# Performance work log

Hardware: AMD Instinct MI355X
Metric: run time of the kernel (lower is better)

## Reference

```python
import jax, jax.numpy as jnp
import numpy as np

T = 11          # entity types
N_ENT = 100000  # entity nodes per type (= NUM_ENTITY_NODES embedding rows)
N_TX = 100000   # transaction nodes (must be <= N_ENT per original code's dst indexing)
D = 128         # hidden_dim (heads=1, concat -> out dim D)
E = 500000      # edges per entity type
F = 394         # tx_feature_dim
NEG_SLOPE = 0.2 # PyG GATConv default
LN_EPS = 1e-5


def _layernorm(x, gamma, beta):
    mu = jnp.mean(x, axis=-1, keepdims=True)
    var = jnp.mean((x - mu) ** 2, axis=-1, keepdims=True)
    return (x - mu) * jax.lax.rsqrt(var + LN_EPS) * gamma + beta


def setup_inputs():
    key = jax.random.key(0)
    ks = jax.random.split(key, 12)
    tx_x = jax.random.normal(ks[0], (N_TX, F), jnp.float32)
    entity_idx = jax.random.randint(ks[1], (T, N_ENT), 0, N_ENT, jnp.int32)
    edge_src = jax.random.randint(ks[2], (T, E), 0, N_ENT, jnp.int32)
    edge_dst = jax.random.randint(ks[3], (T, E), 0, min(N_ENT, N_TX), jnp.int32)
    emb_tables = jax.random.normal(ks[4], (T, N_ENT, D), jnp.float32)
    lin_w = jax.random.normal(ks[5], (D, D), jnp.float32) / np.float32(np.sqrt(D))
    att_src = jax.random.normal(ks[6], (D,), jnp.float32) / np.float32(np.sqrt(D))
    att_dst = jax.random.normal(ks[7], (D,), jnp.float32) / np.float32(np.sqrt(D))
    conv_bias = jnp.zeros((D,), jnp.float32)
    ln_gamma = jnp.ones((T, D), jnp.float32)
    ln_beta = jnp.zeros((T, D), jnp.float32)
    c_in = F + T * D  # classifier input: tx features + 11 entity messages
    w1 = jax.random.normal(ks[8], (c_in, D), jnp.float32) / np.float32(np.sqrt(c_in))
    b1 = jnp.zeros((D,), jnp.float32)
    w2 = jax.random.normal(ks[9], (D, 64), jnp.float32) / np.float32(np.sqrt(D))
    b2 = jnp.zeros((64,), jnp.float32)
    w3 = jax.random.normal(ks[10], (64, 1), jnp.float32) / np.float32(np.sqrt(64))
    b3 = jnp.zeros((1,), jnp.float32)
    return dict(tx_x=tx_x, emb_tables=emb_tables, lin_w=lin_w, att_src=att_src,
                att_dst=att_dst, conv_bias=conv_bias, ln_gamma=ln_gamma, ln_beta=ln_beta,
                w1=w1, b1=b1, w2=w2, b2=b2, w3=w3, b3=b3,
                entity_idx=entity_idx, edge_src=edge_src, edge_dst=edge_dst)


def _forward(tx_x, emb_tables, lin_w, att_src, att_dst, conv_bias, ln_gamma, ln_beta,
             w1, b1, w2, b2, w3, b3, entity_idx, edge_src, edge_dst):
    n_tx = tx_x.shape[0]
    loops = jnp.arange(N_ENT, dtype=edge_src.dtype)  # PyG GATConv add_self_loops=True
    msgs = []
    for t in range(T):  # fixed small set of entity types; GATConv weights shared (convs[0])
        x = emb_tables[t][entity_idx[t]]            # [N_ENT, D] embedding gather
        xw = x @ lin_w                              # GATConv linear (bias=False)
        a_s = xw @ att_src                          # [N_ENT] per-node src attention logit
        a_d = xw @ att_dst
        src, dst = edge_src[t], edge_dst[t]
        s_full = jnp.concatenate([src, loops])      # edges + self loops
        d_full = jnp.concatenate([dst, loops])
        e = jax.nn.leaky_relu(a_s[s_full] + a_d[d_full], NEG_SLOPE)
        # numerically stable edge softmax grouped by dst node
        m = jax.ops.segment_max(e, d_full, num_segments=N_ENT)
        ex = jnp.exp(e - m[d_full])
        denom = jax.ops.segment_sum(ex, d_full, num_segments=N_ENT)
        alpha = ex / (denom[d_full] + 1e-16)
        out = jax.ops.segment_sum(alpha[:, None] * xw[s_full], d_full,
                                  num_segments=N_ENT) + conv_bias  # [N_ENT, D]
        h = _layernorm(out, ln_gamma[t], ln_beta[t])
        # index_add_ scatter of h[src] into transaction rows (original edges only)
        agg = jnp.zeros((n_tx, D), h.dtype).at[dst].add(h[src])
        msgs.append(agg)
    combined = jnp.concatenate([tx_x] + msgs, axis=-1)  # [N_TX, F + T*D]
    h1 = jax.nn.relu(combined @ w1 + b1)
    h2 = jax.nn.relu(h1 @ w2 + b2)
    return h2 @ w3 + b3  # [N_TX, 1] logits


def reference(tx_x, emb_tables, lin_w, att_src, att_dst, conv_bias, ln_gamma, ln_beta,
              w1, b1, w2, b2, w3, b3, entity_idx, edge_src, edge_dst):
    return _forward(tx_x, emb_tables, lin_w, att_src, att_dst, conv_bias, ln_gamma,
                    ln_beta, w1, b1, w2, b2, w3, b3, entity_idx, edge_src, edge_dst)
```

## Files before the change

### kernel.cpp

```cpp
#include <hip/hip_runtime.h>

#define TT 11
#define NE 100000
#define NTX 100000
#define DD 128
#define EE 500000
#define FF 394

__device__ __forceinline__ float leaky(float x) { return x >= 0.f ? x : 0.2f * x; }


__global__ __launch_bounds__(256) void k_init_gemm(
    const float* __restrict__ A, const float* __restrict__ B,
    const float* __restrict__ bias, float* __restrict__ C) {
  __shared__ float As[64][32];
  __shared__ float Bs[32][128];
  int tid = threadIdx.x;
  int ty = tid >> 5, tx = tid & 31;
  int row0 = blockIdx.x * 64;
  float acc[8][4];
  #pragma unroll
  for (int i = 0; i < 8; ++i)
    #pragma unroll
    for (int j = 0; j < 4; ++j) acc[i][j] = 0.f;

  for (int k0 = 0; k0 < FF; k0 += 32) {
    int kc = FF - k0; if (kc > 32) kc = 32;
    for (int idx = tid; idx < 64 * 32; idx += 256) {
      int r = idx >> 5, kk = idx & 31;
      int rg = row0 + r;
      As[r][kk] = (kk < kc && rg < NTX) ? A[(size_t)rg * FF + k0 + kk] : 0.f;
    }
    for (int idx = tid; idx < 32 * 128; idx += 256) {
      int kk = idx >> 7, c = idx & 127;
      Bs[kk][c] = (kk < kc) ? B[(size_t)(k0 + kk) * DD + c] : 0.f;
    }
    __syncthreads();
    for (int kk = 0; kk < 32; ++kk) {
      float4 b = *(float4*)&Bs[kk][tx * 4];
      #pragma unroll
      for (int i = 0; i < 8; ++i) {
        float a = As[ty + 8 * i][kk];
        acc[i][0] = fmaf(a, b.x, acc[i][0]);
        acc[i][1] = fmaf(a, b.y, acc[i][1]);
        acc[i][2] = fmaf(a, b.z, acc[i][2]);
        acc[i][3] = fmaf(a, b.w, acc[i][3]);
      }
    }
    __syncthreads();
  }
  float4 bb = *(const float4*)&bias[tx * 4];
  #pragma unroll
  for (int i = 0; i < 8; ++i) {
    int rg = row0 + ty + 8 * i;
    if (rg < NTX) {
      float4 o = make_float4(acc[i][0] + bb.x, acc[i][1] + bb.y,
                             acc[i][2] + bb.z, acc[i][3] + bb.w);
      *(float4*)&C[(size_t)rg * DD + tx * 4] = o;
    }
  }
}

__global__ __launch_bounds__(256) void k_xw_att(
    const float* __restrict__ emb_t, const int* __restrict__ idx_t,
    const float* __restrict__ B, const float* __restrict__ att_s,
    const float* __restrict__ att_d, float* __restrict__ C,
    float* __restrict__ a_s, float* __restrict__ a_d) {
  __shared__ float As[64][32];
  __shared__ float Bs[32][128];
  __shared__ int sidx[64];
  int tid = threadIdx.x;
  int ty = tid >> 5, tx = tid & 31;
  int row0 = blockIdx.x * 64;
  if (tid < 64) {
    int rg = row0 + tid;
    sidx[tid] = (rg < NE) ? idx_t[rg] : 0;
  }
  __syncthreads();
  float acc[8][4];
  #pragma unroll
  for (int i = 0; i < 8; ++i)
    #pragma unroll
    for (int j = 0; j < 4; ++j) acc[i][j] = 0.f;

  for (int k0 = 0; k0 < DD; k0 += 32) {
    for (int idx = tid; idx < 64 * 32; idx += 256) {
      int r = idx >> 5, kk = idx & 31;
      As[r][kk] = emb_t[(size_t)sidx[r] * DD + k0 + kk];
    }
    for (int idx = tid; idx < 32 * 128; idx += 256) {
      int kk = idx >> 7, c = idx & 127;
      Bs[kk][c] = B[(size_t)(k0 + kk) * DD + c];
    }
    __syncthreads();
    for (int kk = 0; kk < 32; ++kk) {
      float4 b = *(float4*)&Bs[kk][tx * 4];
      #pragma unroll
      for (int i = 0; i < 8; ++i) {
        float a = As[ty + 8 * i][kk];
        acc[i][0] = fmaf(a, b.x, acc[i][0]);
        acc[i][1] = fmaf(a, b.y, acc[i][1]);
        acc[i][2] = fmaf(a, b.z, acc[i][2]);
        acc[i][3] = fmaf(a, b.w, acc[i][3]);
      }
    }
    __syncthreads();
  }
  float4 sv = *(const float4*)&att_s[tx * 4];
  float4 dv = *(const float4*)&att_d[tx * 4];
  #pragma unroll
  for (int i = 0; i < 8; ++i) {
    int rg = row0 + ty + 8 * i;
    float ps = acc[i][0] * sv.x + acc[i][1] * sv.y + acc[i][2] * sv.z + acc[i][3] * sv.w;
    float pd = acc[i][0] * dv.x + acc[i][1] * dv.y + acc[i][2] * dv.z + acc[i][3] * dv.w;
    #pragma unroll
    for (int off = 16; off; off >>= 1) {
      ps += __shfl_xor(ps, off);
      pd += __shfl_xor(pd, off);
    }
    if (rg < NE) {
      *(float4*)&C[(size_t)rg * DD + tx * 4] =
          make_float4(acc[i][0], acc[i][1], acc[i][2], acc[i][3]);
      if (tx == 0) { a_s[rg] = ps; a_d[rg] = pd; }
    }
  }
}

__global__ __launch_bounds__(256) void k_hw_gemm(
    const float* __restrict__ A, const float* __restrict__ B, float* __restrict__ C) {
  __shared__ float As[64][32];
  __shared__ float Bs[32][128];
  int tid = threadIdx.x;
  int ty = tid >> 5, tx = tid & 31;
  int row0 = blockIdx.x * 64;
  float acc[8][4];
  #pragma unroll
  for (int i = 0; i < 8; ++i)
    #pragma unroll
    for (int j = 0; j < 4; ++j) acc[i][j] = 0.f;

  for (int k0 = 0; k0 < DD; k0 += 32) {
    for (int idx = tid; idx < 64 * 32; idx += 256) {
      int r = idx >> 5, kk = idx & 31;
      int rg = row0 + r;
      As[r][kk] = (rg < NE) ? A[(size_t)rg * DD + k0 + kk] : 0.f;
    }
    for (int idx = tid; idx < 32 * 128; idx += 256) {
      int kk = idx >> 7, c = idx & 127;
      Bs[kk][c] = B[(size_t)(k0 + kk) * DD + c];
    }
    __syncthreads();
    for (int kk = 0; kk < 32; ++kk) {
      float4 b = *(float4*)&Bs[kk][tx * 4];
      #pragma unroll
      for (int i = 0; i < 8; ++i) {
        float a = As[ty + 8 * i][kk];
        acc[i][0] = fmaf(a, b.x, acc[i][0]);
        acc[i][1] = fmaf(a, b.y, acc[i][1]);
        acc[i][2] = fmaf(a, b.z, acc[i][2]);
        acc[i][3] = fmaf(a, b.w, acc[i][3]);
      }
    }
    __syncthreads();
  }
  #pragma unroll
  for (int i = 0; i < 8; ++i) {
    int rg = row0 + ty + 8 * i;
    if (rg < NE)
      *(float4*)&C[(size_t)rg * DD + tx * 4] =
          make_float4(acc[i][0], acc[i][1], acc[i][2], acc[i][3]);
  }
}

__global__ void k_hist(const int* __restrict__ dst, int* __restrict__ cnt) {
  int i = blockIdx.x * blockDim.x + threadIdx.x;
  if (i < EE) atomicAdd(&cnt[dst[i]], 1);
}

__global__ __launch_bounds__(256) void k_scan_a(const int* __restrict__ cnt,
                                                int* __restrict__ start,
                                                int* __restrict__ csum) {
  __shared__ int s[256];
  int i = blockIdx.x * 256 + threadIdx.x;
  int v = (i < NE) ? cnt[i] : 0;
  s[threadIdx.x] = v;
  __syncthreads();
  for (int off = 1; off < 256; off <<= 1) {
    int t = (threadIdx.x >= off) ? s[threadIdx.x - off] : 0;
    __syncthreads();
    s[threadIdx.x] += t;
    __syncthreads();
  }
  if (i < NE) start[i] = s[threadIdx.x] - v;
  if (threadIdx.x == 255) csum[blockIdx.x] = s[255];
}

__global__ __launch_bounds__(512) void k_scan_b(int* __restrict__ csum, int n) {
  __shared__ int s[512];
  int v = (threadIdx.x < n) ? csum[threadIdx.x] : 0;
  s[threadIdx.x] = v;
  __syncthreads();
  for (int off = 1; off < 512; off <<= 1) {
    int t = (threadIdx.x >= off) ? s[threadIdx.x - off] : 0;
    __syncthreads();
    s[threadIdx.x] += t;
    __syncthreads();
  }
  if (threadIdx.x < n) csum[threadIdx.x] = s[threadIdx.x] - v;
}

__global__ void k_scan_c(int* __restrict__ start, const int* __restrict__ csum) {
  int i = blockIdx.x * blockDim.x + threadIdx.x;
  if (i < NE) start[i] += csum[blockIdx.x * 256 / 256];
}

__global__ void k_fill(const int* __restrict__ src, const int* __restrict__ dst,
                       int* __restrict__ start, int* __restrict__ eidx) {
  int i = blockIdx.x * blockDim.x + threadIdx.x;
  if (i >= EE) return;
  int p = atomicAdd(&start[dst[i]], 1);
  eidx[p] = src[i];
}

__global__ __launch_bounds__(256) void k_dst_attn(
    const int* __restrict__ start, const int* __restrict__ eidx,
    const float* __restrict__ a_s, const float* __restrict__ a_d,
    const float* __restrict__ xw, const float* __restrict__ cbias,
    const float* __restrict__ gamma, const float* __restrict__ beta,
    float* __restrict__ h) {
  int wid = (blockIdx.x * 256 + threadIdx.x) >> 6;
  int l = threadIdx.x & 63;
  if (wid >= NE) return;
  int d = wid;
  int end = start[d];
  int beg = (d == 0) ? 0 : start[d - 1];
  float ad = a_d[d];
  float eself = leaky(a_s[d] + ad);
  const float2* xw2 = (const float2*)xw;

  float mx = eself;
  for (int base = beg; base < end; base += 64) {
    int i = base + l;
    if (i < end) mx = fmaxf(mx, leaky(a_s[eidx[i]] + ad));
  }
  #pragma unroll
  for (int off = 32; off; off >>= 1) mx = fmaxf(mx, __shfl_xor(mx, off));

  float wself = expf(eself - mx);
  float denom = wself;
  float2 acc;
  float2 xs = xw2[(size_t)d * 64 + l];
  acc.x = wself * xs.x;
  acc.y = wself * xs.y;
  for (int base = beg; base < end; base += 64) {
    int len = end - base; if (len > 64) len = 64;
    int i = base + l;
    int sv = (i < end) ? eidx[i] : 0;
    float av = (i < end) ? a_s[sv] : 0.f;
    for (int j = 0; j < len; ++j) {
      int s = __shfl(sv, j);
      float a = __shfl(av, j);
      float w = expf(leaky(a + ad) - mx);
      denom += w;
      float2 v = xw2[(size_t)s * 64 + l];
      acc.x = fmaf(w, v.x, acc.x);
      acc.y = fmaf(w, v.y, acc.y);
    }
  }
  float inv = 1.f / (denom + 1e-16f);
  float2 cb = ((const float2*)cbias)[l];
  float v0 = acc.x * inv + cb.x;
  float v1 = acc.y * inv + cb.y;

  float s = v0 + v1;
  #pragma unroll
  for (int off = 32; off; off >>= 1) s += __shfl_xor(s, off);
  float mean = s * (1.f / 128.f);
  float d0 = v0 - mean, d1 = v1 - mean;
  float q = d0 * d0 + d1 * d1;
  #pragma unroll
  for (int off = 32; off; off >>= 1) q += __shfl_xor(q, off);
  float r = rsqrtf(q * (1.f / 128.f) + 1e-5f);
  float2 g = ((const float2*)gamma)[l];
  float2 b = ((const float2*)beta)[l];
  float2 o = make_float2(d0 * r * g.x + b.x, d1 * r * g.y + b.y);
  ((float2*)h)[(size_t)d * 64 + l] = o;
}

__global__ __launch_bounds__(256) void k_dst_sum_acc(
    const int* __restrict__ start, const int* __restrict__ eidx,
    const float* __restrict__ hw, float* __restrict__ acc1) {
  int wid = (blockIdx.x * 256 + threadIdx.x) >> 6;
  int l = threadIdx.x & 63;
  if (wid >= NE) return;
  int d = wid;
  int end = start[d];
  int beg = (d == 0) ? 0 : start[d - 1];
  if (beg == end) return;
  const float2* hw2 = (const float2*)hw;
  float2 acc = make_float2(0.f, 0.f);
  for (int base = beg; base < end; base += 64) {
    int len = end - base; if (len > 64) len = 64;
    int i = base + l;
    int sv = (i < end) ? eidx[i] : 0;
    for (int j = 0; j < len; ++j) {
      int s = __shfl(sv, j);
      float2 v = hw2[(size_t)s * 64 + l];
      acc.x += v.x;
      acc.y += v.y;
    }
  }
  float2* p = (float2*)acc1 + (size_t)d * 64 + l;
  float2 old = *p;
  *p = make_float2(old.x + acc.x, old.y + acc.y);
}

__global__ __launch_bounds__(128) void k_tail(
    const float* __restrict__ acc1, const float* __restrict__ w2,
    const float* __restrict__ b2, const float* __restrict__ w3,
    const float* __restrict__ b3, float* __restrict__ out) {
  __shared__ float h1[DD];
  __shared__ float h2s[64];
  int n = blockIdx.x, tid = threadIdx.x;
  float v = acc1[(size_t)n * DD + tid];
  h1[tid] = v > 0.f ? v : 0.f;
  __syncthreads();
  if (tid < 64) {
    float acc = b2[tid];
    for (int k = 0; k < DD; ++k) acc = fmaf(h1[k], w2[k * 64 + tid], acc);
    h2s[tid] = acc > 0.f ? acc : 0.f;
  }
  __syncthreads();
  if (tid < 64) {
    float p = h2s[tid] * w3[tid];
    #pragma unroll
    for (int off = 32; off; off >>= 1) p += __shfl_down(p, off);
    if (tid == 0) out[n] = p + b3[0];
  }
}


extern "C" void kernel_launch(void* const* d_in, const int* in_sizes, int n_in,
                              void* d_out, int out_size, void* d_ws, size_t ws_size,
                              hipStream_t stream) {
  const float* tx_x     = (const float*)d_in[0];
  const float* emb      = (const float*)d_in[1];
  const float* lin_w    = (const float*)d_in[2];
  const float* att_src  = (const float*)d_in[3];
  const float* att_dst  = (const float*)d_in[4];
  const float* conv_bias= (const float*)d_in[5];
  const float* ln_gamma = (const float*)d_in[6];
  const float* ln_beta  = (const float*)d_in[7];
  const float* w1       = (const float*)d_in[8];
  const float* b1       = (const float*)d_in[9];
  const float* w2       = (const float*)d_in[10];
  const float* b2       = (const float*)d_in[11];
  const float* w3       = (const float*)d_in[12];
  const float* b3       = (const float*)d_in[13];
  const int* entity_idx = (const int*)d_in[14];
  const int* edge_src   = (const int*)d_in[15];
  const int* edge_dst   = (const int*)d_in[16];
  float* out = (float*)d_out;

  float* ws   = (float*)d_ws;
  float* acc1 = ws;
  float* xw   = acc1 + (size_t)NTX * DD;
  float* h    = xw + (size_t)NE * DD;
  float* a_s  = h + (size_t)NE * DD;
  float* a_d  = a_s + NE;
  int* start  = (int*)(a_d + NE);
  int* eidx   = start + NE;
  int* cnt    = (int*)h;
  int* csum   = cnt + 102400;
  float* hw   = xw;

  const int NBLK = (NE + 255) / 256;
  const int GROWS = (NE + 63) / 64;

  k_init_gemm<<<(NTX + 63) / 64, 256, 0, stream>>>(tx_x, w1, b1, acc1);

  for (int t = 0; t < TT; ++t) {
    const float* emb_t = emb + (size_t)t * NE * DD;
    const int* idx_t   = entity_idx + (size_t)t * NE;
    const int* src     = edge_src + (size_t)t * EE;
    const int* dst     = edge_dst + (size_t)t * EE;
    const float* gamma = ln_gamma + t * DD;
    const float* beta  = ln_beta + t * DD;
    const float* w1t   = w1 + (size_t)(FF + t * DD) * DD;

    k_xw_att<<<GROWS, 256, 0, stream>>>(emb_t, idx_t, lin_w, att_src, att_dst,
                                        xw, a_s, a_d);
    hipMemsetAsync(cnt, 0, NE * sizeof(int), stream);
    k_hist<<<(EE + 255) / 256, 256, 0, stream>>>(dst, cnt);
    k_scan_a<<<NBLK, 256, 0, stream>>>(cnt, start, csum);
    k_scan_b<<<1, 512, 0, stream>>>(csum, NBLK);
    k_scan_c<<<NBLK, 256, 0, stream>>>(start, csum);
    k_fill<<<(EE + 255) / 256, 256, 0, stream>>>(src, dst, start, eidx);
    k_dst_attn<<<(NE + 3) / 4, 256, 0, stream>>>(start, eidx, a_s, a_d, xw,
                                                 conv_bias, gamma, beta, h);
    k_hw_gemm<<<GROWS, 256, 0, stream>>>(h, w1t, hw);
    k_dst_sum_acc<<<(NE + 3) / 4, 256, 0, stream>>>(start, eidx, hw, acc1);
  }

  k_tail<<<NTX, DD, 0, stream>>>(acc1, w2, b2, w3, b3, out);
}
```

Before: 4.674 ms.

## Use 128x128 register-tiled GEMMs and batch CSR build across all entity types

The three fp32 GEMM kernels move from 64-row tiles with 8x4 outputs per thread to 128-row tiles with 8x8 outputs per thread. They use vectorized float4 global loads and a transposed, padded A tile in shared memory, so each k step needs fewer shared-memory reads per FMA. The histogram, scan and fill stages that build the dst-sorted edge lists now run once for all 11 types using a 2D grid, when the workspace is large enough. This removes many small launches and memsets from the per-type loop. In exchange, register pressure rises with 64 accumulators per thread, and the batched path needs extra workspace for per-type start and eidx arrays.

Measured after the change: 4.393 ms. 6.0% less time.

```diff
diff --git a/kernel.cpp b/kernel.cpp
--- a/kernel.cpp
+++ b/kernel.cpp
@@ -6,6 +6,7 @@
 #define DD 128
 #define EE 500000
 #define FF 394
+#define NBLK 391
 
 __device__ __forceinline__ float leaky(float x) { return x >= 0.f ? x : 0.2f * x; }
 
@@ -13,50 +14,74 @@
 __global__ __launch_bounds__(256) void k_init_gemm(
     const float* __restrict__ A, const float* __restrict__ B,
     const float* __restrict__ bias, float* __restrict__ C) {
-  __shared__ float As[64][32];
+  __shared__ float As[32][132];
   __shared__ float Bs[32][128];
   int tid = threadIdx.x;
-  int ty = tid >> 5, tx = tid & 31;
-  int row0 = blockIdx.x * 64;
-  float acc[8][4];
+  int tx = tid & 15, ty = tid >> 4;
+  int row0 = blockIdx.x * 128;
+  int lkq = tid & 7, lr = tid >> 3;
+  int lc4 = tid & 31, lkb = tid >> 5;
+  float acc[8][8];
   #pragma unroll
   for (int i = 0; i < 8; ++i)
     #pragma unroll
-    for (int j = 0; j < 4; ++j) acc[i][j] = 0.f;
+    for (int j = 0; j < 8; ++j) acc[i][j] = 0.f;
 
   for (int k0 = 0; k0 < FF; k0 += 32) {
-    int kc = FF - k0; if (kc > 32) kc = 32;
-    for (int idx = tid; idx < 64 * 32; idx += 256) {
-      int r = idx >> 5, kk = idx & 31;
+    #pragma unroll
+    for (int p = 0; p < 4; ++p) {
+      int r = lr + 32 * p;
       int rg = row0 + r;
-      As[r][kk] = (kk < kc && rg < NTX) ? A[(size_t)rg * FF + k0 + kk] : 0.f;
-    }
-    for (int idx = tid; idx < 32 * 128; idx += 256) {
-      int kk = idx >> 7, c = idx & 127;
-      Bs[kk][c] = (kk < kc) ? B[(size_t)(k0 + kk) * DD + c] : 0.f;
-    }
-    __syncthreads();
+      int kg = k0 + 4 * lkq;
+      float4 v = make_float4(0.f, 0.f, 0.f, 0.f);
+      if (rg < NTX) {
+        const float* ap = A + (size_t)rg * FF;
+        if (kg + 3 < FF) v = *(const float4*)(ap + kg);
+        else {
+          if (kg < FF) v.x = ap[kg];
+          if (kg + 1 < FF) v.y = ap[kg + 1];
+          if (kg + 2 < FF) v.z = ap[kg + 2];
+        }
+      }
+      As[4 * lkq + 0][r] = v.x; As[4 * lkq + 1][r] = v.y;
+      As[4 * lkq + 2][r] = v.z; As[4 * lkq + 3][r] = v.w;
+    }
+    #pragma unroll
+    for (int p = 0; p < 4; ++p) {
+      int kk = lkb + 8 * p;
+      int kg = k0 + kk;
+      float4 v = make_float4(0.f, 0.f, 0.f, 0.f);
+      if (kg < FF) v = *(const float4*)&B[(size_t)kg * DD + 4 * lc4];
+      *(float4*)&Bs[kk][4 * lc4] = v;
+    }
+    __syncthreads();
+    #pragma unroll
     for (int kk = 0; kk < 32; ++kk) {
-      float4 b = *(float4*)&Bs[kk][tx * 4];
+      float4 a0 = *(float4*)&As[kk][8 * ty];
+      float4 a1 = *(float4*)&As[kk][8 * ty + 4];
+      float4 b0 = *(float4*)&Bs[kk][4 * tx];
+      float4 b1 = *(float4*)&Bs[kk][64 + 4 * tx];
+      float av[8] = {a0.x, a0.y, a0.z, a0.w, a1.x, a1.y, a1.z, a1.w};
+      float bv[8] = {b0.x, b0.y, b0.z, b0.w, b1.x, b1.y, b1.z, b1.w};
       #pragma unroll
-      for (int i = 0; i < 8; ++i) {
-        float a = As[ty + 8 * i][kk];
-        acc[i][0] = fmaf(a, b.x, acc[i][0]);
-        acc[i][1] = fmaf(a, b.y, acc[i][1]);
-        acc[i][2] = fmaf(a, b.z, acc[i][2]);
-        acc[i][3] = fmaf(a, b.w, acc[i][3]);
-      }
-    }
-    __syncthreads();
-  }
-  float4 bb = *(const float4*)&bias[tx * 4];
+      for (int i = 0; i < 8; ++i)
+        #pragma unroll
+        for (int j = 0; j < 8; ++j) acc[i][j] = fmaf(av[i], bv[j], acc[i][j]);
+    }
+    __syncthreads();
+  }
+  float4 bb0 = *(const float4*)&bias[4 * tx];
+  float4 bb1 = *(const float4*)&bias[64 + 4 * tx];
   #pragma unroll
   for (int i = 0; i < 8; ++i) {
-    int rg = row0 + ty + 8 * i;
+    int rg = row0 + 8 * ty + i;
     if (rg < NTX) {
-      float4 o = make_float4(acc[i][0] + bb.x, acc[i][1] + bb.y,
-                             acc[i][2] + bb.z, acc[i][3] + bb.w);
-      *(float4*)&C[(size_t)rg * DD + tx * 4] = o;
+      float4 o0 = make_float4(acc[i][0] + bb0.x, acc[i][1] + bb0.y,
+                              acc[i][2] + bb0.z, acc[i][3] + bb0.w);
+      float4 o1 = make_float4(acc[i][4] + bb1.x, acc[i][5] + bb1.y,
+                              acc[i][6] + bb1.z, acc[i][7] + bb1.w);
+      *(float4*)&C[(size_t)rg * DD + 4 * tx] = o0;
+      *(float4*)&C[(size_t)rg * DD + 64 + 4 * tx] = o1;
     }
   }
 }
@@ -66,61 +91,77 @@
     const float* __restrict__ B, const float* __restrict__ att_s,
     const float* __restrict__ att_d, float* __restrict__ C,
     float* __restrict__ a_s, float* __restrict__ a_d) {
-  __shared__ float As[64][32];
+  __shared__ float As[32][132];
   __shared__ float Bs[32][128];
-  __shared__ int sidx[64];
+  __shared__ int sidx[128];
   int tid = threadIdx.x;
-  int ty = tid >> 5, tx = tid & 31;
-  int row0 = blockIdx.x * 64;
-  if (tid < 64) {
+  int tx = tid & 15, ty = tid >> 4;
+  int row0 = blockIdx.x * 128;
+  int lkq = tid & 7, lr = tid >> 3;
+  int lc4 = tid & 31, lkb = tid >> 5;
+  if (tid < 128) {
     int rg = row0 + tid;
     sidx[tid] = (rg < NE) ? idx_t[rg] : 0;
   }
   __syncthreads();
-  float acc[8][4];
+  float acc[8][8];
   #pragma unroll
   for (int i = 0; i < 8; ++i)
     #pragma unroll
-    for (int j = 0; j < 4; ++j) acc[i][j] = 0.f;
+    for (int j = 0; j < 8; ++j) acc[i][j] = 0.f;
 
   for (int k0 = 0; k0 < DD; k0 += 32) {
-    for (int idx = tid; idx < 64 * 32; idx += 256) {
-      int r = idx >> 5, kk = idx & 31;
-      As[r][kk] = emb_t[(size_t)sidx[r] * DD + k0 + kk];
-    }
-    for (int idx = tid; idx < 32 * 128; idx += 256) {
-      int kk = idx >> 7, c = idx & 127;
-      Bs[kk][c] = B[(size_t)(k0 + kk) * DD + c];
-    }
-    __syncthreads();
+    #pragma unroll
+    for (int p = 0; p < 4; ++p) {
+      int r = lr + 32 * p;
+      int kg = k0 + 4 * lkq;
+      float4 v = *(const float4*)(emb_t + (size_t)sidx[r] * DD + kg);
+      As[4 * lkq + 0][r] = v.x; As[4 * lkq + 1][r] = v.y;
+      As[4 * lkq + 2][r] = v.z; As[4 * lkq + 3][r] = v.w;
+    }
+    #pragma unroll
+    for (int p = 0; p < 4; ++p) {
+      int kk = lkb + 8 * p;
+      float4 v = *(const float4*)&B[(size_t)(k0 + kk) * DD + 4 * lc4];
+      *(float4*)&Bs[kk][4 * lc4] = v;
+    }
+    __syncthreads();
+    #pragma unroll
     for (int kk = 0; kk < 32; ++kk) {
-      float4 b = *(float4*)&Bs[kk][tx * 4];
+      float4 a0 = *(float4*)&As[kk][8 * ty];
+      float4 a1 = *(float4*)&As[kk][8 * ty + 4];
+      float4 b0 = *(float4*)&Bs[kk][4 * tx];
+      float4 b1 = *(float4*)&Bs[kk][64 + 4 * tx];
+      float av[8] = {a0.x, a0.y, a0.z, a0.w, a1.x, a1.y, a1.z, a1.w};
+      float bv[8] = {b0.x, b0.y, b0.z, b0.w, b1.x, b1.y, b1.z, b1.w};
       #pragma unroll
-      for (int i = 0; i < 8; ++i) {
-        float a = As[ty + 8 * i][kk];
-        acc[i][0] = fmaf(a, b.x, acc[i][0]);
-        acc[i][1] = fmaf(a, b.y, acc[i][1]);
-        acc[i][2] = fmaf(a, b.z, acc[i][2]);
-        acc[i][3] = fmaf(a, b.w, acc[i][3]);
-      }
-    }
-    __syncthreads();
-  }
-  float4 sv = *(const float4*)&att_s[tx * 4];
-  float4 dv = *(const float4*)&att_d[tx * 4];
+      for (int i = 0; i < 8; ++i)
+        #pragma unroll
+        for (int j = 0; j < 8; ++j) acc[i][j] = fmaf(av[i], bv[j], acc[i][j]);
+    }
+    __syncthreads();
+  }
+  float4 sv0 = *(const float4*)&att_s[4 * tx];
+  float4 sv1 = *(const float4*)&att_s[64 + 4 * tx];
+  float4 dv0 = *(const float4*)&att_d[4 * tx];
+  float4 dv1 = *(const float4*)&att_d[64 + 4 * tx];
   #pragma unroll
   for (int i = 0; i < 8; ++i) {
-    int rg = row0 + ty + 8 * i;
-    float ps = acc[i][0] * sv.x + acc[i][1] * sv.y + acc[i][2] * sv.z + acc[i][3] * sv.w;
-    float pd = acc[i][0] * dv.x + acc[i][1] * dv.y + acc[i][2] * dv.z + acc[i][3] * dv.w;
-    #pragma unroll
-    for (int off = 16; off; off >>= 1) {
+    int rg = row0 + 8 * ty + i;
+    float ps = acc[i][0] * sv0.x + acc[i][1] * sv0.y + acc[i][2] * sv0.z + acc[i][3] * sv0.w
+             + acc[i][4] * sv1.x + acc[i][5] * sv1.y + acc[i][6] * sv1.z + acc[i][7] * sv1.w;
+    float pd = acc[i][0] * dv0.x + acc[i][1] * dv0.y + acc[i][2] * dv0.z + acc[i][3] * dv0.w
+             + acc[i][4] * dv1.x + acc[i][5] * dv1.y + acc[i][6] * dv1.z + acc[i][7] * dv1.w;
+    #pragma unroll
+    for (int off = 8; off; off >>= 1) {
       ps += __shfl_xor(ps, off);
       pd += __shfl_xor(pd, off);
     }
     if (rg < NE) {
-      *(float4*)&C[(size_t)rg * DD + tx * 4] =
+      *(float4*)&C[(size_t)rg * DD + 4 * tx] =
           make_float4(acc[i][0], acc[i][1], acc[i][2], acc[i][3]);
+      *(float4*)&C[(size_t)rg * DD + 64 + 4 * tx] =
+          make_float4(acc[i][4], acc[i][5], acc[i][6], acc[i][7]);
       if (tx == 0) { a_s[rg] = ps; a_d[rg] = pd; }
     }
   }
@@ -128,98 +169,117 @@
 
 __global__ __launch_bounds__(256) void k_hw_gemm(
     const float* __restrict__ A, const float* __restrict__ B, float* __restrict__ C) {
-  __shared__ float As[64][32];
+  __shared__ float As[32][132];
   __shared__ float Bs[32][128];
   int tid = threadIdx.x;
-  int ty = tid >> 5, tx = tid & 31;
-  int row0 = blockIdx.x * 64;
-  float acc[8][4];
+  int tx = tid & 15, ty = tid >> 4;
+  int row0 = blockIdx.x * 128;
+  int lkq = tid & 7, lr = tid >> 3;
+  int lc4 = tid & 31, lkb = tid >> 5;
+  float acc[8][8];
   #pragma unroll
   for (int i = 0; i < 8; ++i)
     #pragma unroll
-    for (int j = 0; j < 4; ++j) acc[i][j] = 0.f;
+    for (int j = 0; j < 8; ++j) acc[i][j] = 0.f;
 
   for (int k0 = 0; k0 < DD; k0 += 32) {
-    for (int idx = tid; idx < 64 * 32; idx += 256) {
-      int r = idx >> 5, kk = idx & 31;
+    #pragma unroll
+    for (int p = 0; p < 4; ++p) {
+      int r = lr + 32 * p;
       int rg = row0 + r;
-      As[r][kk] = (rg < NE) ? A[(size_t)rg * DD + k0 + kk] : 0.f;
-    }
-    for (int idx = tid; idx < 32 * 128; idx += 256) {
-      int kk = idx >> 7, c = idx & 127;
-      Bs[kk][c] = B[(size_t)(k0 + kk) * DD + c];
-    }
-    __syncthreads();
+      int kg = k0 + 4 * lkq;
+      float4 v = make_float4(0.f, 0.f, 0.f, 0.f);
+      if (rg < NE) v = *(const float4*)(A + (size_t)rg * DD + kg);
+      As[4 * lkq + 0][r] = v.x; As[4 * lkq + 1][r] = v.y;
+      As[4 * lkq + 2][r] = v.z; As[4 * lkq + 3][r] = v.w;
+    }
+    #pragma unroll
+    for (int p = 0; p < 4; ++p) {
+      int kk = lkb + 8 * p;
+      float4 v = *(const float4*)&B[(size_t)(k0 + kk) * DD + 4 * lc4];
+      *(float4*)&Bs[kk][4 * lc4] = v;
+    }
+    __syncthreads();
+    #pragma unroll
     for (int kk = 0; kk < 32; ++kk) {
-      float4 b = *(float4*)&Bs[kk][tx * 4];
+      float4 a0 = *(float4*)&As[kk][8 * ty];
+      float4 a1 = *(float4*)&As[kk][8 * ty + 4];
+      float4 b0 = *(float4*)&Bs[kk][4 * tx];
+      float4 b1 = *(float4*)&Bs[kk][64 + 4 * tx];
+      float av[8] = {a0.x, a0.y, a0.z, a0.w, a1.x, a1.y, a1.z, a1.w};
+      float bv[8] = {b0.x, b0.y, b0.z, b0.w, b1.x, b1.y, b1.z, b1.w};
       #pragma unroll
-      for (int i = 0; i < 8; ++i) {
-        float a = As[ty + 8 * i][kk];
-        acc[i][0] = fmaf(a, b.x, acc[i][0]);
-        acc[i][1] = fmaf(a, b.y, acc[i][1]);
-        acc[i][2] = fmaf(a, b.z, acc[i][2]);
-        acc[i][3] = fmaf(a, b.w, acc[i][3]);
-      }
+      for (int i = 0; i < 8; ++i)
+        #pragma unroll
+        for (int j = 0; j < 8; ++j) acc[i][j] = fmaf(av[i], bv[j], acc[i][j]);
     }
     __syncthreads();
   }
   #pragma unroll
   for (int i = 0; i < 8; ++i) {
-    int rg = row0 + ty + 8 * i;
-    if (rg < NE)
-      *(float4*)&C[(size_t)rg * DD + tx * 4] =
+    int rg = row0 + 8 * ty + i;
+    if (rg < NE) {
+      *(float4*)&C[(size_t)rg * DD + 4 * tx] =
           make_float4(acc[i][0], acc[i][1], acc[i][2], acc[i][3]);
-  }
-}
-
-__global__ void k_hist(const int* __restrict__ dst, int* __restrict__ cnt) {
-  int i = blockIdx.x * blockDim.x + threadIdx.x;
-  if (i < EE) atomicAdd(&cnt[dst[i]], 1);
+      *(float4*)&C[(size_t)rg * DD + 64 + 4 * tx] =
+          make_float4(acc[i][4], acc[i][5], acc[i][6], acc[i][7]);
+    }
+  }
+}
+
+__global__ void k_hist(const int* __restrict__ dst_all, int* __restrict__ cnt_all) {
+  int t = blockIdx.y;
+  int i = blockIdx.x * 256 + threadIdx.x;
+  if (i < EE) atomicAdd(&cnt_all[(size_t)t * NE + dst_all[(size_t)t * EE + i]], 1);
 }
 
 __global__ __launch_bounds__(256) void k_scan_a(const int* __restrict__ cnt,
                                                 int* __restrict__ start,
                                                 int* __restrict__ csum) {
   __shared__ int s[256];
+  int t = blockIdx.y;
   int i = blockIdx.x * 256 + threadIdx.x;
-  int v = (i < NE) ? cnt[i] : 0;
+  int v = (i < NE) ? cnt[(size_t)t * NE + i] : 0;
   s[threadIdx.x] = v;
   __syncthreads();
   for (int off = 1; off < 256; off <<= 1) {
-    int t = (threadIdx.x >= off) ? s[threadIdx.x - off] : 0;
-    __syncthreads();
-    s[threadIdx.x] += t;
-    __syncthreads();
-  }
-  if (i < NE) start[i] = s[threadIdx.x] - v;
-  if (threadIdx.x == 255) csum[blockIdx.x] = s[255];
-}
-
-__global__ __launch_bounds__(512) void k_scan_b(int* __restrict__ csum, int n) {
+    int u = (threadIdx.x >= off) ? s[threadIdx.x - off] : 0;
+    __syncthreads();
+    s[threadIdx.x] += u;
+    __syncthreads();
+  }
+  if (i < NE) start[(size_t)t * NE + i] = s[threadIdx.x] - v;
+  if (threadIdx.x == 255) csum[t * NBLK + blockIdx.x] = s[255];
+}
+
+__global__ __launch_bounds__(512) void k_scan_b(int* __restrict__ csum) {
   __shared__ int s[512];
-  int v = (threadIdx.x < n) ? csum[threadIdx.x] : 0;
+  int t = blockIdx.y;
+  int v = (threadIdx.x < NBLK) ? csum[t * NBLK + threadIdx.x] : 0;
   s[threadIdx.x] = v;
   __syncthreads();
   for (int off = 1; off < 512; off <<= 1) {
-    int t = (threadIdx.x >= off) ? s[threadIdx.x - off] : 0;
-    __syncthreads();
-    s[threadIdx.x] += t;
-    __syncthreads();
-  }
-  if (threadIdx.x < n) csum[threadIdx.x] = s[threadIdx.x] - v;
+    int u = (threadIdx.x >= off) ? s[threadIdx.x - off] : 0;
+    __syncthreads();
+    s[threadIdx.x] += u;
+    __syncthreads();
+  }
+  if (threadIdx.x < NBLK) csum[t * NBLK + threadIdx.x] = s[threadIdx.x] - v;
 }
 
 __global__ void k_scan_c(int* __restrict__ start, const int* __restrict__ csum) {
-  int i = blockIdx.x * blockDim.x + threadIdx.x;
-  if (i < NE) start[i] += csum[blockIdx.x * 256 / 256];
-}
-
-__global__ void k_fill(const int* __restrict__ src, const int* __restrict__ dst,
+  int t = blockIdx.y;
+  int i = blockIdx.x * 256 + threadIdx.x;
+  if (i < NE) start[(size_t)t * NE + i] += csum[t * NBLK + blockIdx.x];
+}
+
+__global__ void k_fill(const int* __restrict__ src_all, const int* __restrict__ dst_all,
                        int* __restrict__ start, int* __restrict__ eidx) {
-  int i = blockIdx.x * blockDim.x + threadIdx.x;
+  int t = blockIdx.y;
+  int i = blockIdx.x * 256 + threadIdx.x;
   if (i >= EE) return;
-  int p = atomicAdd(&start[dst[i]], 1);
-  eidx[p] = src[i];
+  int p = atomicAdd(&start[(size_t)t * NE + dst_all[(size_t)t * EE + i]], 1);
+  eidx[(size_t)t * EE + p] = src_all[(size_t)t * EE + i];
 }
 
 __global__ __launch_bounds__(256) void k_dst_attn(
@@ -368,38 +428,76 @@
   float* h    = xw + (size_t)NE * DD;
   float* a_s  = h + (size_t)NE * DD;
   float* a_d  = a_s + NE;
-  int* start  = (int*)(a_d + NE);
-  int* eidx   = start + NE;
-  int* cnt    = (int*)h;
-  int* csum   = cnt + 102400;
+  int* start_base = (int*)(a_d + NE);
   float* hw   = xw;
 
-  const int NBLK = (NE + 255) / 256;
-  const int GROWS = (NE + 63) / 64;
-
-  k_init_gemm<<<(NTX + 63) / 64, 256, 0, stream>>>(tx_x, w1, b1, acc1);
-
-  for (int t = 0; t < TT; ++t) {
-    const float* emb_t = emb + (size_t)t * NE * DD;
-    const int* idx_t   = entity_idx + (size_t)t * NE;
-    const int* src     = edge_src + (size_t)t * EE;
-    const int* dst     = edge_dst + (size_t)t * EE;
-    const float* gamma = ln_gamma + t * DD;
-    const float* beta  = ln_beta + t * DD;
-    const float* w1t   = w1 + (size_t)(FF + t * DD) * DD;
-
-    k_xw_att<<<GROWS, 256, 0, stream>>>(emb_t, idx_t, lin_w, att_src, att_dst,
-                                        xw, a_s, a_d);
-    hipMemsetAsync(cnt, 0, NE * sizeof(int), stream);
-    k_hist<<<(EE + 255) / 256, 256, 0, stream>>>(dst, cnt);
-    k_scan_a<<<NBLK, 256, 0, stream>>>(cnt, start, csum);
-    k_scan_b<<<1, 512, 0, stream>>>(csum, NBLK);
-    k_scan_c<<<NBLK, 256, 0, stream>>>(start, csum);
-    k_fill<<<(EE + 255) / 256, 256, 0, stream>>>(src, dst, start, eidx);
-    k_dst_attn<<<(NE + 3) / 4, 256, 0, stream>>>(start, eidx, a_s, a_d, xw,
-                                                 conv_bias, gamma, beta, h);
-    k_hw_gemm<<<GROWS, 256, 0, stream>>>(h, w1t, hw);
-    k_dst_sum_acc<<<(NE + 3) / 4, 256, 0, stream>>>(start, eidx, hw, acc1);
+  size_t base_floats = (size_t)NTX * DD + 2 * (size_t)NE * DD + 2 * (size_t)NE;
+  size_t need_batched = base_floats * sizeof(float)
+                      + ((size_t)TT * NE + (size_t)TT * EE) * sizeof(int);
+  bool batched = ws_size >= need_batched;
+
+  const int GB = (NE + 127) / 128;
+  const int EB = (EE + 255) / 256;
+
+  k_init_gemm<<<(NTX + 127) / 128, 256, 0, stream>>>(tx_x, w1, b1, acc1);
+
+  if (batched) {
+    int* start_all = start_base;
+    int* eidx_all  = start_all + (size_t)TT * NE;
+    int* cnt_all   = (int*)h;
+    int* csum      = cnt_all + (size_t)TT * NE;
+
+    hipMemsetAsync(cnt_all, 0, (size_t)TT * NE * sizeof(int), stream);
+    k_hist<<<dim3(EB, TT), 256, 0, stream>>>(edge_dst, cnt_all);
+    k_scan_a<<<dim3(NBLK, TT), 256, 0, stream>>>(cnt_all, start_all, csum);
+    k_scan_b<<<dim3(1, TT), 512, 0, stream>>>(csum);
+    k_scan_c<<<dim3(NBLK, TT), 256, 0, stream>>>(start_all, csum);
+    k_fill<<<dim3(EB, TT), 256, 0, stream>>>(edge_src, edge_dst, start_all, eidx_all);
+
+    for (int t = 0; t < TT; ++t) {
+      const float* emb_t = emb + (size_t)t * NE * DD;
+      const int* idx_t   = entity_idx + (size_t)t * NE;
+      const float* gamma = ln_gamma + t * DD;
+      const float* beta  = ln_beta + t * DD;
+      const float* w1t   = w1 + (size_t)(FF + t * DD) * DD;
+      const int* start_t = start_all + (size_t)t * NE;
+      const int* eidx_t  = eidx_all + (size_t)t * EE;
+
+      k_xw_att<<<GB, 256, 0, stream>>>(emb_t, idx_t, lin_w, att_src, att_dst,
+                                       xw, a_s, a_d);
+      k_dst_attn<<<(NE + 3) / 4, 256, 0, stream>>>(start_t, eidx_t, a_s, a_d, xw,
+                                                   conv_bias, gamma, beta, h);
+      k_hw_gemm<<<GB, 256, 0, stream>>>(h, w1t, hw);
+      k_dst_sum_acc<<<(NE + 3) / 4, 256, 0, stream>>>(start_t, eidx_t, hw, acc1);
+    }
+  } else {
+    int* start = start_base;
+    int* eidx  = start + NE;
+    int* cnt   = (int*)h;
+    int* csum  = cnt + (size_t)NE;
+
+    for (int t = 0; t < TT; ++t) {
+      const float* emb_t = emb + (size_t)t * NE * DD;
+      const int* idx_t   = entity_idx + (size_t)t * NE;
+      const int* src     = edge_src + (size_t)t * EE;
+      const int* dst     = edge_dst + (size_t)t * EE;
+      const float* gamma = ln_gamma + t * DD;
+      const float* beta  = ln_beta + t * DD;
+      const float* w1t   = w1 + (size_t)(FF + t * DD) * DD;
+
+      k_xw_att<<<GB, 256, 0, stream>>>(emb_t, idx_t, lin_w, att_src, att_dst,
+                                       xw, a_s, a_d);
+      hipMemsetAsync(cnt, 0, NE * sizeof(int), stream);
+      k_hist<<<dim3(EB, 1), 256, 0, stream>>>(dst, cnt);
+      k_scan_a<<<dim3(NBLK, 1), 256, 0, stream>>>(cnt, start, csum);
+      k_scan_b<<<dim3(1, 1), 512, 0, stream>>>(csum);
+      k_scan_c<<<dim3(NBLK, 1), 256, 0, stream>>>(start, csum);
+      k_fill<<<dim3(EB, 1), 256, 0, stream>>>(src, dst, start, eidx);
+      k_dst_attn<<<(NE + 3) / 4, 256, 0, stream>>>(start, eidx, a_s, a_d, xw,
+                                                   conv_bias, gamma, beta, h);
+      k_hw_gemm<<<GB, 256, 0, stream>>>(h, w1t, hw);
+      k_dst_sum_acc<<<(NE + 3) / 4, 256, 0, stream>>>(start, eidx, hw, acc1);
+    }
   }
 
   k_tail<<<NTX, DD, 0, stream>>>(acc1, w2, b2, w3, b3, out);
```
